# Kernel tuning notes

Measured on AMD Instinct MI355X. Metric: run time of the kernel, lower is better.

## Reference

```python
import jax, jax.numpy as jnp
import numpy as np

DIM = 1024
HEADS = 8
EV = DIM  # dim*expand - dim with expand=2
P = 2.0   # power-softmax exponent
EPS = 1e-5


def setup_inputs() -> dict:
    key = jax.random.key(0)
    k1, k2, k3 = jax.random.split(key, 3)
    B, L = 4, 2048
    x = jax.random.normal(k1, (B, L, DIM), dtype=jnp.float32)
    gamma = jnp.ones((DIM,), dtype=jnp.float32)
    beta = jnp.zeros((DIM,), dtype=jnp.float32)
    # torch nn.Linear weights are [out_features, in_features]
    w_qkv = jax.random.normal(k2, (5 * DIM, DIM), dtype=jnp.float32) * (DIM ** -0.5)
    w_out = jax.random.normal(k3, (DIM, 2 * DIM), dtype=jnp.float32) * ((2 * DIM) ** -0.5)
    return {"x": x, "gamma": gamma, "beta": beta, "w_qkv": w_qkv, "w_out": w_out}


def _layernorm(x, gamma, beta):
    xf = x.astype(jnp.float32)
    mu = jnp.mean(xf, axis=-1, keepdims=True)
    var = jnp.mean(jnp.square(xf - mu), axis=-1, keepdims=True)
    return ((xf - mu) * jax.lax.rsqrt(var + EPS)) * gamma + beta


def _p_softmax(scores, scale, p):
    # scores: [B,H,L,L] with -inf on masked entries
    s = scores.astype(jnp.float32) * scale
    if p == 1.0:
        return jax.nn.softmax(s, axis=-1)
    lse = jax.nn.logsumexp(s * p, axis=-1, keepdims=True) / p
    return jnp.exp(s - lse)


def _attention(q, k, v, heads, p):
    B, L, D = q.shape
    hd = D // heads
    q = q.reshape(B, L, heads, hd).transpose(0, 2, 1, 3)  # bhld
    k = k.reshape(B, L, heads, hd).transpose(0, 2, 1, 3)
    v = v.reshape(B, L, heads, hd).transpose(0, 2, 1, 3)
    scores = jnp.einsum('bhqd,bhkd->bhqk', q, k)
    mask = jnp.tril(jnp.ones((L, L), dtype=bool))
    scores = jnp.where(mask, scores, -jnp.inf)
    probs = _p_softmax(scores, hd ** -0.5, p).astype(q.dtype)
    out = jnp.einsum('bhqk,bhkd->bhqd', probs, v)
    return out.transpose(0, 2, 1, 3).reshape(B, L, D)


def reference(x, gamma, beta, w_qkv, w_out):
    h = _layernorm(x, gamma, beta).astype(x.dtype)
    proj = h @ w_qkv.T  # [B,L,5*DIM]
    q, k, v, lin, pre = jnp.split(proj, np.cumsum([DIM, DIM, DIM, EV]), axis=-1)
    attn = _attention(q, k, v, HEADS, P)
    branch = jnp.concatenate([lin * jax.nn.gelu(pre, approximate=False), attn], axis=-1)
    return x + branch @ w_out.T
```

## Files before the change

### kernel.cpp

```cpp
#include <hip/hip_runtime.h>
#include <hip/hip_bf16.h>
#include <math.h>

#define DIMD 1024
#define LSEQ 2048
#define BATCH 4
#define NHEAD 8
#define HD 128
#define NROWS (BATCH*LSEQ)
#define PROJC (5*DIMD)
#define BRC (2*DIMD)

typedef __attribute__((ext_vector_type(8))) short short8;
typedef __attribute__((ext_vector_type(4))) short short4v;
typedef __attribute__((ext_vector_type(4))) float floatx4;

__device__ __forceinline__ float bf2f(short s) {
  unsigned int u = ((unsigned int)(unsigned short)s) << 16;
  return __builtin_bit_cast(float, u);
}
__device__ __forceinline__ short f2bf(float f) {
  unsigned int u = __builtin_bit_cast(unsigned int, f);
  unsigned int lsb = (u >> 16) & 1u;
  u += 0x7fffu + lsb;
  return (short)(u >> 16);
}

__device__ __forceinline__ void gl2lds16(const short* g, short* l) {
  __builtin_amdgcn_global_load_lds(
      (const __attribute__((address_space(1))) unsigned int*)(unsigned long long)g,
      (__attribute__((address_space(3))) unsigned int*)(unsigned int)(unsigned long long)l,
      16, 0, 0);
}

__global__ __launch_bounds__(256) void cvt2_kernel(const float* __restrict__ s1,
    short* __restrict__ d1, int n1_4, const float* __restrict__ s2,
    short* __restrict__ d2, int n2_4) {
  int i = blockIdx.x * 256 + threadIdx.x;
  const float* src; short* dst;
  if (i < n1_4) { src = s1; dst = d1; }
  else { i -= n1_4; if (i >= n2_4) return; src = s2; dst = d2; }
  float4 v = *(const float4*)(src + (size_t)i * 4);
  short4v o;
  o[0] = f2bf(v.x); o[1] = f2bf(v.y); o[2] = f2bf(v.z); o[3] = f2bf(v.w);
  *(short4v*)(dst + (size_t)i * 4) = o;
}

__global__ __launch_bounds__(256) void ln_kernel(const float* __restrict__ x,
    const float* __restrict__ gamma, const float* __restrict__ beta,
    short* __restrict__ h) {
  int row = blockIdx.x;
  int c = threadIdx.x * 4;
  const float* xr = x + (size_t)row * DIMD;
  float4 v = *(const float4*)(xr + c);
  float f[4] = {v.x, v.y, v.z, v.w};
  float sum = 0.f, sq = 0.f;
  for (int i = 0; i < 4; ++i) { sum += f[i]; sq += f[i]*f[i]; }
  for (int off = 1; off < 64; off <<= 1) {
    sum += __shfl_xor(sum, off);
    sq  += __shfl_xor(sq, off);
  }
  __shared__ float red[8];
  int wid = threadIdx.x >> 6;
  if ((threadIdx.x & 63) == 0) { red[wid*2] = sum; red[wid*2+1] = sq; }
  __syncthreads();
  sum = red[0]+red[2]+red[4]+red[6];
  sq  = red[1]+red[3]+red[5]+red[7];
  float mu = sum * (1.0f/DIMD);
  float var = sq * (1.0f/DIMD) - mu*mu;
  float rstd = rsqrtf(var + 1e-5f);
  float4 g = *(const float4*)(gamma + c);
  float4 bb = *(const float4*)(beta + c);
  float gg[4] = {g.x, g.y, g.z, g.w};
  float bv[4] = {bb.x, bb.y, bb.z, bb.w};
  short4v o;
  for (int i = 0; i < 4; ++i)
    o[i] = f2bf((f[i] - mu) * rstd * gg[i] + bv[i]);
  *(short4v*)(h + (size_t)row * DIMD + c) = o;
}

template<int MODE>
__global__ __launch_bounds__(256) void gemm_bt(const short* __restrict__ A,
    const short* __restrict__ W, const float* __restrict__ X,
    void* __restrict__ Cv, int M, int N, int K) {
  __shared__ __align__(16) short As[128*64];
  __shared__ __align__(16) short Ws[128*64];
  int tid = threadIdx.x;
  int row0 = blockIdx.y * 128;
  int col0 = blockIdx.x * 128;
  int lane = tid & 63, wv = tid >> 6;
  int wr = (wv >> 1) * 64, wc = (wv & 1) * 64;
  int quad = lane >> 4, l16 = lane & 15;
  floatx4 acc[4][4] = {};
  int srow = lane >> 3;
  int gq = ((lane & 7) - srow) & 7;
  const short* Ag = A + (size_t)(row0 + wv*8 + srow) * K + gq*8;
  const short* Wg = W + (size_t)(col0 + wv*8 + srow) * K + gq*8;
  short* Al = As + wv*8*64;
  short* Wl = Ws + wv*8*64;
  int qsr0 = (((quad)     + (l16 & 7)) & 7) * 8;
  int qsr1 = (((quad + 4) + (l16 & 7)) & 7) * 8;
  for (int k0 = 0; k0 < K; k0 += 64) {
    __syncthreads();
    for (int c = 0; c < 4; ++c) {
      gl2lds16(Ag + k0 + (size_t)(c*32)*K, Al + c*32*64);
      gl2lds16(Wg + k0 + (size_t)(c*32)*K, Wl + c*32*64);
    }
    __syncthreads();
    short8 af[4], wf[4];
    for (int i = 0; i < 4; ++i) af[i] = *(const short8*)&As[(wr + i*16 + l16)*64 + qsr0];
    for (int j = 0; j < 4; ++j) wf[j] = *(const short8*)&Ws[(wc + j*16 + l16)*64 + qsr0];
    for (int i = 0; i < 4; ++i)
      for (int j = 0; j < 4; ++j)
        acc[i][j] = __builtin_amdgcn_mfma_f32_16x16x32_bf16(af[i], wf[j], acc[i][j], 0, 0, 0);
    for (int i = 0; i < 4; ++i) af[i] = *(const short8*)&As[(wr + i*16 + l16)*64 + qsr1];
    for (int j = 0; j < 4; ++j) wf[j] = *(const short8*)&Ws[(wc + j*16 + l16)*64 + qsr1];
    for (int i = 0; i < 4; ++i)
      for (int j = 0; j < 4; ++j)
        acc[i][j] = __builtin_amdgcn_mfma_f32_16x16x32_bf16(af[i], wf[j], acc[i][j], 0, 0, 0);
  }
  for (int i = 0; i < 4; ++i) {
    int r0 = row0 + wr + i*16 + quad*4;
    for (int j = 0; j < 4; ++j) {
      int cc = col0 + wc + j*16 + l16;
      for (int r = 0; r < 4; ++r) {
        float v = acc[i][j][r];
        size_t idx = (size_t)(r0 + r) * N + cc;
        if (MODE == 0) {
          ((short*)Cv)[idx] = f2bf(v);
        } else {
          ((float*)Cv)[idx] = v + X[idx];
        }
      }
    }
  }
}

__global__ __launch_bounds__(256) void gelu_kernel(const short* __restrict__ proj,
    short* __restrict__ branch) {
  int row = blockIdx.x;
  int c = threadIdx.x * 4;
  const short* pr = proj + (size_t)row * PROJC;
  short4v lin = *(const short4v*)(pr + 3*DIMD + c);
  short4v pre = *(const short4v*)(pr + 4*DIMD + c);
  short4v o;
  for (int i = 0; i < 4; ++i) {
    float xx = bf2f(pre[i]);
    float g = 0.5f * xx * (1.f + erff(xx * 0.70710678118654752f));
    o[i] = f2bf(bf2f(lin[i]) * g);
  }
  *(short4v*)(branch + (size_t)row * BRC + c) = o;
}

__global__ __launch_bounds__(256) void vt_kernel(const short* __restrict__ proj,
    short* __restrict__ vt) {
  int bh = blockIdx.y;
  int b = bh >> 3, hh = bh & 7;
  int l0 = blockIdx.x * 64;
  __shared__ short Ls[64][136];
  int tid = threadIdx.x;
  int r = tid >> 4, c = (tid & 15) * 8;
  const short* Vp = proj + (size_t)b * LSEQ * PROJC + 2*DIMD + hh*HD;
  for (int p = 0; p < 4; ++p)
    *(short8*)&Ls[r + p*16][c] = *(const short8*)(Vp + (size_t)(l0 + r + p*16) * PROJC + c);
  __syncthreads();
  int d = tid >> 1, lh = (tid & 1) * 32;
  short* outp = vt + ((size_t)bh * HD + d) * LSEQ + l0 + lh;
  for (int g = 0; g < 4; ++g) {
    short8 o;
    for (int j = 0; j < 8; ++j) o[j] = Ls[lh + g*8 + j][d];
    *(short8*)(outp + g*8) = o;
  }
}

__global__ __launch_bounds__(512) void attn_kernel(const short* __restrict__ proj,
    const short* __restrict__ vt, short* __restrict__ branch) {
  int bh = blockIdx.y;
  int b = bh >> 3, hh = bh & 7;
  int bid = blockIdx.x;
  int tid = threadIdx.x;
  int wv = tid >> 6, lane = tid & 63, quad = lane >> 4, l16 = lane & 15;
  int qsel = (wv < 4) ? bid : (31 - bid);
  int qw = qsel * 64 + (wv & 3) * 16;

  const short* Qp  = proj + (size_t)b * LSEQ * PROJC + hh*HD;
  const short* Kp  = Qp + DIMD;
  const short* VTp = vt + (size_t)bh * HD * LSEQ;

  __shared__ short Ks[64][136];
  __shared__ short Vs[128][76];
  __shared__ short Ps[8][16][44];

  short8 qf[4];
  {
    const short* qrow = Qp + (size_t)(qw + l16) * PROJC;
    for (int s = 0; s < 4; ++s) qf[s] = *(const short8*)(qrow + s*32 + quad*8);
  }
  float lsum[4] = {0.f, 0.f, 0.f, 0.f};
  floatx4 O[8] = {};

  const float scale = 0.08838834764831845f;
  int NT = 32 - bid;
  int krow = tid >> 4;
  int kcol = (tid & 15) * 8;
  int vd = tid >> 2;
  int vk = (tid & 3) * 8;
  for (int kt = 0; kt < NT; ++kt) {
    int kb64 = kt * 64;
    short8 kv0 = *(const short8*)(Kp + (size_t)(kb64 + krow) * PROJC + kcol);
    short8 kv1 = *(const short8*)(Kp + (size_t)(kb64 + 32 + krow) * PROJC + kcol);
    short8 vv0 = *(const short8*)(VTp + (size_t)vd * LSEQ + kb64 + vk);
    short8 vv1 = *(const short8*)(VTp + (size_t)vd * LSEQ + kb64 + 32 + vk);
    __syncthreads();
    *(short8*)&Ks[krow][kcol]      = kv0;
    *(short8*)&Ks[krow + 32][kcol] = kv1;
    *(short8*)&Vs[vd][vk]          = vv0;
    *(short8*)&Vs[vd][32 + vk]     = vv1;
    __syncthreads();
    for (int hf = 0; hf < 2; ++hf) {
      int kb = kb64 + hf*32;
      if (kb <= qw + 15) {
        floatx4 s0 = {0.f,0.f,0.f,0.f}, s1 = {0.f,0.f,0.f,0.f};
        for (int s = 0; s < 4; ++s) {
          short8 kf0 = *(const short8*)&Ks[hf*32 + l16][s*32 + quad*8];
          short8 kf1 = *(const short8*)&Ks[hf*32 + 16 + l16][s*32 + quad*8];
          s0 = __builtin_amdgcn_mfma_f32_16x16x32_bf16(qf[s], kf0, s0, 0, 0, 0);
          s1 = __builtin_amdgcn_mfma_f32_16x16x32_bf16(qf[s], kf1, s1, 0, 0, 0);
        }
        int c0 = kb + l16, c1 = kb + 16 + l16;
        for (int r = 0; r < 4; ++r) {
          int q = qw + quad*4 + r;
          float w0 = (c0 <= q) ? __expf(s0[r] * scale) : 0.f;
          float w1 = (c1 <= q) ? __expf(s1[r] * scale) : 0.f;
          lsum[r] += w0*w0 + w1*w1;
          Ps[wv][quad*4+r][l16]      = f2bf(w0);
          Ps[wv][quad*4+r][16 + l16] = f2bf(w1);
        }
        asm volatile("s_waitcnt lgkmcnt(0)" ::: "memory");
        short8 pf = *(const short8*)&Ps[wv][l16][quad*8];
        for (int t8 = 0; t8 < 8; ++t8) {
          short8 vf = *(const short8*)&Vs[t8*16 + l16][hf*32 + quad*8];
          O[t8] = __builtin_amdgcn_mfma_f32_16x16x32_bf16(pf, vf, O[t8], 0, 0, 0);
        }
      }
    }
  }
  for (int r = 0; r < 4; ++r) {
    float l = lsum[r];
    for (int off = 1; off < 16; off <<= 1) l += __shfl_xor(l, off);
    float inv = rsqrtf(l);
    int q = qw + quad*4 + r;
    short* orow = branch + ((size_t)(b*LSEQ + q)) * BRC + DIMD + hh*HD;
    for (int t8 = 0; t8 < 8; ++t8)
      orow[t8*16 + l16] = f2bf(O[t8][r] * inv);
  }
}

extern "C" void kernel_launch(void* const* d_in, const int* in_sizes, int n_in,
                              void* d_out, int out_size, void* d_ws, size_t ws_size,
                              hipStream_t stream) {
  const float* x     = (const float*)d_in[0];
  const float* gamma = (const float*)d_in[1];
  const float* beta  = (const float*)d_in[2];
  const float* w_qkv = (const float*)d_in[3];
  const float* w_out = (const float*)d_in[4];
  float* out = (float*)d_out;

  char* ws = (char*)d_ws;
  short* h      = (short*)ws;
  short* proj   = (short*)(ws + (size_t)16*1024*1024);
  short* branch = (short*)(ws + (size_t)96*1024*1024);
  short* wq     = (short*)(ws + (size_t)128*1024*1024);
  short* wo     = (short*)(ws + (size_t)138*1024*1024);
  short* vt     = h;

  int n1 = PROJC*DIMD/4, n2 = DIMD*BRC/4;
  cvt2_kernel<<<(n1 + n2 + 255)/256, 256, 0, stream>>>(w_qkv, wq, n1, w_out, wo, n2);
  ln_kernel<<<NROWS, 256, 0, stream>>>(x, gamma, beta, h);
  gemm_bt<0><<<dim3(PROJC/128, NROWS/128), 256, 0, stream>>>(h, wq, nullptr, proj,
                                                             NROWS, PROJC, DIMD);
  gelu_kernel<<<NROWS, 256, 0, stream>>>(proj, branch);
  vt_kernel<<<dim3(LSEQ/64, BATCH*NHEAD), 256, 0, stream>>>(proj, vt);
  attn_kernel<<<dim3(16, BATCH*NHEAD), 512, 0, stream>>>(proj, vt, branch);
  gemm_bt<1><<<dim3(DIMD/128, NROWS/128), 256, 0, stream>>>(branch, wo, x, out,
                                                            NROWS, DIMD, BRC);
}
```

Baseline: 358.9 us.

## Replace QKV projection GEMM with 256x256-tile ping-pong pipelined kernel

Adds a new 256x256-tile bf16 GEMM using 512 threads, double-buffered LDS filled by direct global-to-LDS loads, and an interleaved schedule of LDS reads, MFMAs and prefetches separated by workgroup barriers with raised priority during MFMA. It also remaps the block index into an XCD-aware order so neighbouring tiles share cache. It replaces the 128x128 tile kernel for the QKV projection, aiming for more data reuse per tile and better overlap of memory with compute. The trade-offs are larger LDS use, fewer blocks on the grid, and reliance on many explicit barriers and waitcnts being correct.

```diff
diff --git a/kernel.cpp b/kernel.cpp
--- a/kernel.cpp
+++ b/kernel.cpp
@@ -31,6 +31,15 @@
       (const __attribute__((address_space(1))) unsigned int*)(unsigned long long)g,
       (__attribute__((address_space(3))) unsigned int*)(unsigned int)(unsigned long long)l,
       16, 0, 0);
+}
+
+__device__ __forceinline__ void wgbar() {
+  asm volatile("" ::: "memory");
+  __builtin_amdgcn_s_barrier();
+  asm volatile("" ::: "memory");
+}
+__device__ __forceinline__ void lgkm0() {
+  asm volatile("s_waitcnt lgkmcnt(0)" ::: "memory");
 }
 
 __global__ __launch_bounds__(256) void cvt2_kernel(const float* __restrict__ s1,
@@ -77,6 +86,144 @@
   for (int i = 0; i < 4; ++i)
     o[i] = f2bf((f[i] - mu) * rstd * gg[i] + bv[i]);
   *(short4v*)(h + (size_t)row * DIMD + c) = o;
+}
+
+
+__device__ __forceinline__ void rd_a(const short* base, int s0, int s1,
+                                     short8 (&a)[4][2]) {
+#pragma unroll
+  for (int m = 0; m < 4; ++m) {
+    a[m][0] = *(const short8*)(base + m*16*64 + s0);
+    a[m][1] = *(const short8*)(base + m*16*64 + s1);
+  }
+}
+__device__ __forceinline__ void rd_b(const short* base, int s0, int s1,
+                                     short8 (&b)[2][2]) {
+#pragma unroll
+  for (int n = 0; n < 2; ++n) {
+    b[n][0] = *(const short8*)(base + n*16*64 + s0);
+    b[n][1] = *(const short8*)(base + n*16*64 + s1);
+  }
+}
+template<int QM, int QN>
+__device__ __forceinline__ void qmm(const short8 (&a)[4][2], const short8 (&b)[2][2],
+                                    floatx4 (&acc)[8][4]) {
+  __builtin_amdgcn_s_setprio(1);
+#pragma unroll
+  for (int m = 0; m < 4; ++m)
+#pragma unroll
+    for (int n = 0; n < 2; ++n) {
+      floatx4 c = acc[QM*4+m][QN*2+n];
+      c = __builtin_amdgcn_mfma_f32_16x16x32_bf16(a[m][0], b[n][0], c, 0, 0, 0);
+      c = __builtin_amdgcn_mfma_f32_16x16x32_bf16(a[m][1], b[n][1], c, 0, 0, 0);
+      acc[QM*4+m][QN*2+n] = c;
+    }
+  __builtin_amdgcn_s_setprio(0);
+}
+__device__ __forceinline__ void stg2(const short* p, int K, short* lds) {
+  gl2lds16(p, lds);
+  gl2lds16(p + (size_t)64*K, lds + 64*64);
+}
+__device__ __forceinline__ void stg4(const short* p, int K, short* lds, int koff) {
+  stg2(p + koff, K, lds);
+  stg2(p + (size_t)128*K + koff, K, lds + 128*64);
+}
+
+__global__ __launch_bounds__(512, 2) void gemm256(const short* __restrict__ A,
+    const short* __restrict__ W, short* __restrict__ C, int M, int N, int K) {
+  __shared__ __align__(16) short AsF[2*256*64];
+  __shared__ __align__(16) short WsF[2*256*64];
+  const int tid = threadIdx.x;
+  const int lane = tid & 63, wv = tid >> 6;
+  const int wm = wv >> 2, wn = wv & 3;
+  const int quad = lane >> 4, l16 = lane & 15;
+
+  const int nbx = N >> 8;
+  int cpx = gridDim.x >> 3;
+  int orig = blockIdx.x;
+  int wg = (orig & 7) * cpx + (orig >> 3);
+  int bx = wg % nbx, by = wg / nbx;
+  const int row0 = by << 8, col0 = bx << 8;
+
+  const int lrow = lane >> 3;
+  const int sslot = (lane & 7) ^ lrow;
+  const short* pA = A + (size_t)(row0 + wv*8 + lrow) * K + sslot*8;
+  const short* pW = W + (size_t)(col0 + wv*8 + lrow) * K + sslot*8;
+  short* stA = AsF + wv*8*64;
+  short* stW = WsF + wv*8*64;
+  const short* aB = AsF + (wm*128 + l16)*64;
+  const short* wB = WsF + (wn*64 + l16)*64;
+  const int s0 = (quad ^ (l16 & 7)) << 3;
+  const int s1 = s0 ^ 32;
+
+  floatx4 acc[8][4] = {};
+  short8 a[4][2], b0[2][2], b1[2][2];
+
+  const int nktm = (K >> 6) - 1;
+
+  stg4(pA, K, stA, 0);
+  stg4(pW, K, stW, 0);
+  stg4(pA, K, stA + 16384, 64);
+  asm volatile("s_waitcnt vmcnt(4)" ::: "memory");
+  wgbar();
+
+  const int NIT = K >> 7;
+  for (int it = 0; it < NIT; ++it) {
+    const int kb1 = (2*it + 1) << 6;
+    const int k2  = ((2*it + 2) & nktm) << 6;
+    const int k3  = ((2*it + 3) & nktm) << 6;
+    rd_a(aB, s0, s1, a);
+    rd_b(wB, s0, s1, b0);
+    stg4(pW, K, stW + 16384, kb1);
+    wgbar(); lgkm0();
+    qmm<0,0>(a, b0, acc);
+    wgbar();
+    rd_b(wB + 32*64, s0, s1, b1);
+    wgbar(); lgkm0();
+    qmm<0,1>(a, b1, acc);
+    wgbar();
+    rd_a(aB + 64*64, s0, s1, a);
+    wgbar(); lgkm0();
+    qmm<1,1>(a, b1, acc);
+    wgbar();
+    stg4(pA, K, stA, k2);
+    wgbar();
+    qmm<1,0>(a, b0, acc);
+    asm volatile("s_waitcnt vmcnt(4)" ::: "memory");
+    wgbar();
+    rd_a(aB + 16384, s0, s1, a);
+    rd_b(wB + 16384, s0, s1, b0);
+    stg4(pW, K, stW, k2);
+    wgbar(); lgkm0();
+    qmm<0,0>(a, b0, acc);
+    wgbar();
+    rd_b(wB + 16384 + 32*64, s0, s1, b1);
+    wgbar(); lgkm0();
+    qmm<0,1>(a, b1, acc);
+    wgbar();
+    rd_a(aB + 16384 + 64*64, s0, s1, a);
+    wgbar(); lgkm0();
+    qmm<1,1>(a, b1, acc);
+    wgbar();
+    stg4(pA, K, stA + 16384, k3);
+    wgbar();
+    qmm<1,0>(a, b0, acc);
+    asm volatile("s_waitcnt vmcnt(4)" ::: "memory");
+    wgbar();
+  }
+  asm volatile("s_waitcnt vmcnt(0)" ::: "memory");
+
+#pragma unroll
+  for (int i = 0; i < 8; ++i) {
+    int r0 = row0 + wm*128 + i*16 + quad*4;
+#pragma unroll
+    for (int j = 0; j < 4; ++j) {
+      int cc = col0 + wn*64 + j*16 + l16;
+#pragma unroll
+      for (int r = 0; r < 4; ++r)
+        C[(size_t)(r0 + r) * N + cc] = f2bf(acc[i][j][r]);
+    }
+  }
 }
 
 template<int MODE>
@@ -277,7 +424,7 @@
   int n1 = PROJC*DIMD/4, n2 = DIMD*BRC/4;
   cvt2_kernel<<<(n1 + n2 + 255)/256, 256, 0, stream>>>(w_qkv, wq, n1, w_out, wo, n2);
   ln_kernel<<<NROWS, 256, 0, stream>>>(x, gamma, beta, h);
-  gemm_bt<0><<<dim3(PROJC/128, NROWS/128), 256, 0, stream>>>(h, wq, nullptr, proj,
+  gemm256<<<dim3((NROWS/256)*(PROJC/256)), 512, 0, stream>>>(h, wq, proj,
                                                              NROWS, PROJC, DIMD);
   gelu_kernel<<<NROWS, 256, 0, stream>>>(proj, branch);
   vt_kernel<<<dim3(LSEQ/64, BATCH*NHEAD), 256, 0, stream>>>(proj, vt);
```

Result: no change. 356.5 us (-0.7%).
